# Performance work log

Measured on AMD Instinct MI355X. Metric: run time of the kernel, lower is better.

## Reference

```python
import jax, jax.numpy as jnp
import numpy as np

N = 100000   # nodes
E = 1600000  # edges (avg degree 16)
D = 128      # input channels
H = 128      # hidden channels
BN_EPS = 1e-5

def setup_inputs() -> dict:
    key = jax.random.key(0)
    ks = jax.random.split(key, 8)
    x = jax.random.normal(ks[0], (N, D), dtype=jnp.float32)
    edge_index = jax.random.randint(ks[1], (2, E), 0, N, dtype=jnp.int32)
    s = 0.02
    W1 = jax.random.normal(ks[2], (D, H), dtype=jnp.float32) * s
    b1 = jnp.zeros((H,), jnp.float32)
    g1 = jnp.ones((H,), jnp.float32)   # BN gamma
    be1 = jnp.zeros((H,), jnp.float32) # BN beta
    W2 = jax.random.normal(ks[3], (H, H), dtype=jnp.float32) * s
    b2 = jnp.zeros((H,), jnp.float32)
    g2 = jnp.ones((H,), jnp.float32)
    be2 = jnp.zeros((H,), jnp.float32)
    eps = jnp.zeros((), jnp.float32)   # trainable GIN eps, init 0
    return {"x": x, "edge_index": edge_index, "W1": W1, "b1": b1, "g1": g1,
            "be1": be1, "W2": W2, "b2": b2, "g2": g2, "be2": be2, "eps": eps}

def _bn_relu(h, gamma, beta):
    # BatchNorm1d in training mode: biased batch statistics over the node dim
    mu = jnp.mean(h, axis=0)
    var = jnp.mean(jnp.square(h - mu), axis=0)
    return jax.nn.relu((h - mu) * jax.lax.rsqrt(var + BN_EPS) * gamma + beta)

def reference(x, edge_index, W1, b1, g1, be1, W2, b2, g2, be2, eps):
    src, dst = edge_index[0], edge_index[1]
    # GIN neighbor aggregation: scatter-add of source features onto destinations
    agg = jax.ops.segment_sum(x[src], dst, num_segments=x.shape[0])  # [N, D]
    h = (1.0 + eps) * x + agg
    # 2-layer MLP: Linear -> BN -> ReLU, twice
    h = _bn_relu(h @ W1 + b1, g1, be1)
    h = _bn_relu(h @ W2 + b2, g2, be2)
    return h
```

## Files before the change

### kernel.cpp

```cpp
#include <hip/hip_runtime.h>

#define DIM 128
#define BINSHIFT 7
#define BINSZ 128
#define BCAP 2560
#define EPB 8192

typedef __attribute__((ext_vector_type(8))) short bf16x8;
typedef __attribute__((ext_vector_type(4))) float f32x4;

__device__ inline unsigned short f2b(float f) {
    unsigned u = __builtin_bit_cast(unsigned, f);
    unsigned r = (u + 0x7FFFu + ((u >> 16) & 1u)) >> 16;
    return (unsigned short)r;
}
__device__ inline float b2f(unsigned short h) {
    unsigned u = ((unsigned)h) << 16;
    return __builtin_bit_cast(float, u);
}

__global__ __launch_bounds__(256)
void x_to_bf16z(const float* __restrict__ x, unsigned short* __restrict__ xb,
                unsigned* __restrict__ zbuf, int n8)
{
    if (blockIdx.x == 0) {
        #pragma unroll
        for (int q = 0; q < 6; ++q) zbuf[threadIdx.x + q * 256] = 0u;
    }
    int i = blockIdx.x * 256 + threadIdx.x;
    if (i >= n8) return;
    float4 a = ((const float4*)x)[i * 2];
    float4 b = ((const float4*)x)[i * 2 + 1];
    bf16x8 o;
    o[0] = (short)f2b(a.x); o[1] = (short)f2b(a.y); o[2] = (short)f2b(a.z); o[3] = (short)f2b(a.w);
    o[4] = (short)f2b(b.x); o[5] = (short)f2b(b.y); o[6] = (short)f2b(b.z); o[7] = (short)f2b(b.w);
    ((bf16x8*)xb)[i] = o;
}

__global__ __launch_bounds__(1024)
void bin_edges(const int* __restrict__ src, const int* __restrict__ dst,
               unsigned* __restrict__ gcur, unsigned* __restrict__ binned,
               int E, int nbins)
{
    __shared__ unsigned hist[1024];
    __shared__ unsigned base[1024];
    const int t = threadIdx.x;
    const long long bb = (long long)blockIdx.x * EPB;
    if (t < nbins) hist[t] = 0;
    __syncthreads();

    unsigned pk[8], pos[8];
    int bn[8];
    bool ok[8];
    #pragma unroll
    for (int i = 0; i < 8; ++i) {
        long long idx = bb + i * 1024 + t;
        ok[i] = idx < E;
        if (ok[i]) {
            int s = src[idx], d = dst[idx];
            pk[i] = ((unsigned)(d & (BINSZ - 1)) << 17) | (unsigned)s;
            bn[i] = d >> BINSHIFT;
            pos[i] = atomicAdd(&hist[bn[i]], 1u);
        }
    }
    __syncthreads();
    if (t < nbins) base[t] = (unsigned)t * BCAP + atomicAdd(&gcur[t], hist[t]);
    __syncthreads();
    #pragma unroll
    for (int i = 0; i < 8; ++i) {
        if (ok[i]) {
            unsigned off = base[bn[i]] + pos[i];
            if (off < (unsigned)(bn[i] + 1) * BCAP) binned[off] = pk[i];
        }
    }
}

__global__ __launch_bounds__(512)
void bin_sort(const unsigned* __restrict__ gcur, const unsigned* __restrict__ binned,
              unsigned* __restrict__ srt, unsigned* __restrict__ gbase,
              unsigned* __restrict__ ghist)
{
    __shared__ unsigned hist[BINSZ];
    __shared__ unsigned base[BINSZ];
    __shared__ unsigned cur[BINSZ];
    const int t = threadIdx.x;
    const int bin = blockIdx.x;

    if (t < BINSZ) hist[t] = 0;
    __syncthreads();

    int cnt = (int)gcur[bin];
    if (cnt > BCAP) cnt = BCAP;
    const unsigned* __restrict__ bp = binned + (size_t)bin * BCAP;

    for (int i = t; i < cnt; i += 512)
        atomicAdd(&hist[(bp[i] >> 17) & (BINSZ - 1)], 1u);
    __syncthreads();
    if (t == 0) {
        unsigned run = 0;
        for (int i = 0; i < BINSZ; ++i) { base[i] = run; run += hist[i]; }
    }
    __syncthreads();
    if (t < BINSZ) cur[t] = base[t];
    __syncthreads();
    unsigned* __restrict__ sp = srt + (size_t)bin * BCAP;
    for (int i = t; i < cnt; i += 512) {
        unsigned p = bp[i];
        unsigned pos = atomicAdd(&cur[(p >> 17) & (BINSZ - 1)], 1u);
        sp[pos] = p & 0x1FFFFu;
    }
    if (t < BINSZ) {
        gbase[bin * BINSZ + t] = base[t];
        ghist[bin * BINSZ + t] = hist[t];
    }
}

__global__ __launch_bounds__(512)
void gather_csr(const unsigned short* __restrict__ xb, const float* __restrict__ epsp,
                const unsigned* __restrict__ srt, const unsigned* __restrict__ gbase,
                const unsigned* __restrict__ ghist,
                unsigned short* __restrict__ h0b, int N)
{
    const int t = threadIdx.x;
    const int node = blockIdx.x * 32 + (t >> 4);
    if (node >= N) return;
    const int g = (t & 15) * 8;
    const float e = 1.0f + epsp[0];

    bf16x8 v0 = *(const bf16x8*)(xb + (size_t)node * DIM + g);
    float acc[8];
    #pragma unroll
    for (int q = 0; q < 8; ++q) acc[q] = e * b2f((unsigned short)v0[q]);

    const int b0 = (int)gbase[node];
    const int hn = (int)ghist[node];
    const unsigned* __restrict__ sp = srt + (size_t)(node >> BINSHIFT) * BCAP + b0;

    int j = 0;
    for (; j + 8 <= hn; j += 8) {
        unsigned s0 = sp[j+0], s1 = sp[j+1], s2 = sp[j+2], s3 = sp[j+3];
        unsigned s4 = sp[j+4], s5 = sp[j+5], s6 = sp[j+6], s7 = sp[j+7];
        bf16x8 r0 = *(const bf16x8*)(xb + (size_t)s0 * DIM + g);
        bf16x8 r1 = *(const bf16x8*)(xb + (size_t)s1 * DIM + g);
        bf16x8 r2 = *(const bf16x8*)(xb + (size_t)s2 * DIM + g);
        bf16x8 r3 = *(const bf16x8*)(xb + (size_t)s3 * DIM + g);
        bf16x8 r4 = *(const bf16x8*)(xb + (size_t)s4 * DIM + g);
        bf16x8 r5 = *(const bf16x8*)(xb + (size_t)s5 * DIM + g);
        bf16x8 r6 = *(const bf16x8*)(xb + (size_t)s6 * DIM + g);
        bf16x8 r7 = *(const bf16x8*)(xb + (size_t)s7 * DIM + g);
        #pragma unroll
        for (int q = 0; q < 8; ++q)
            acc[q] += b2f((unsigned short)r0[q]) + b2f((unsigned short)r1[q])
                    + b2f((unsigned short)r2[q]) + b2f((unsigned short)r3[q])
                    + b2f((unsigned short)r4[q]) + b2f((unsigned short)r5[q])
                    + b2f((unsigned short)r6[q]) + b2f((unsigned short)r7[q]);
    }
    for (; j + 2 <= hn; j += 2) {
        unsigned s0 = sp[j+0], s1 = sp[j+1];
        bf16x8 r0 = *(const bf16x8*)(xb + (size_t)s0 * DIM + g);
        bf16x8 r1 = *(const bf16x8*)(xb + (size_t)s1 * DIM + g);
        #pragma unroll
        for (int q = 0; q < 8; ++q)
            acc[q] += b2f((unsigned short)r0[q]) + b2f((unsigned short)r1[q]);
    }
    for (; j < hn; ++j) {
        unsigned s0 = sp[j];
        bf16x8 r0 = *(const bf16x8*)(xb + (size_t)s0 * DIM + g);
        #pragma unroll
        for (int q = 0; q < 8; ++q) acc[q] += b2f((unsigned short)r0[q]);
    }
    bf16x8 o;
    #pragma unroll
    for (int q = 0; q < 8; ++q) o[q] = (short)f2b(acc[q]);
    *(bf16x8*)(h0b + (size_t)node * DIM + g) = o;
}

template<bool APPLY_BN, bool OUT_BF16>
__global__ __launch_bounds__(1024)
void gemm_mfma(const unsigned short* __restrict__ A, const float* __restrict__ Wf,
               const float* __restrict__ bias,
               const float* __restrict__ stats_in, const float* __restrict__ gamma,
               const float* __restrict__ beta, float invN,
               void* __restrict__ outp, float* __restrict__ stats, int N)
{
    __shared__ unsigned short sWT[128 * 128];
    __shared__ float red[256];
    __shared__ float sss[256];
    const int tid = threadIdx.x;

    if (APPLY_BN && tid < 128) {
        float mu  = stats_in[tid] * invN;
        float var = fmaxf(stats_in[128 + tid] * invN - mu * mu, 0.f);
        float sc  = gamma[tid] * rsqrtf(var + 1e-5f);
        sss[tid]       = sc;
        sss[128 + tid] = beta[tid] - mu * sc;
    }
    #pragma unroll
    for (int i = 0; i < 4; ++i) {
        int idx = (i * 1024 + tid) * 4;
        float4 w = *(const float4*)&Wf[idx];
        int k = idx >> 7, n0 = idx & 127;
        sWT[(n0 + 0) * 128 + (k ^ (((n0 + 0) & 7) << 3))] = f2b(w.x);
        sWT[(n0 + 1) * 128 + (k ^ (((n0 + 1) & 7) << 3))] = f2b(w.y);
        sWT[(n0 + 2) * 128 + (k ^ (((n0 + 2) & 7) << 3))] = f2b(w.z);
        sWT[(n0 + 3) * 128 + (k ^ (((n0 + 3) & 7) << 3))] = f2b(w.w);
    }
    if (tid < 256) red[tid] = 0.f;
    __syncthreads();

    const int lane = tid & 63;
    const int wave = tid >> 6;
    const int r0   = blockIdx.x * 256 + wave * 16;
    const int rl   = lane & 15;
    const int kg   = lane >> 4;
    int rr = r0 + rl;
    int rclamp = rr < N ? rr : N - 1;
    const unsigned short* arow = A + (size_t)rclamp * DIM + kg * 8;

    f32x4 acc[8];
    #pragma unroll
    for (int nt = 0; nt < 8; ++nt) acc[nt] = (f32x4)(0.f);

    #pragma unroll
    for (int kk = 0; kk < 128; kk += 32) {
        bf16x8 a8 = *(const bf16x8*)(arow + kk);
        if (APPLY_BN) {
            const int cb = kk + kg * 8;
            bf16x8 tt;
            #pragma unroll
            for (int j = 0; j < 8; ++j) {
                float f = b2f((unsigned short)a8[j]) * sss[cb + j] + sss[128 + cb + j];
                tt[j] = (short)f2b(fmaxf(f, 0.f));
            }
            a8 = tt;
        }
        const int ks = kk + kg * 8;
        #pragma unroll
        for (int nt = 0; nt < 8; ++nt) {
            int n = nt * 16 + rl;
            bf16x8 b8 = *(const bf16x8*)&sWT[n * 128 + (ks ^ ((n & 7) << 3))];
            acc[nt] = __builtin_amdgcn_mfma_f32_16x16x32_bf16(a8, b8, acc[nt], 0, 0, 0);
        }
    }

    const int orow0 = r0 + kg * 4;
    #pragma unroll
    for (int nt = 0; nt < 8; ++nt) {
        int n = nt * 16 + rl;
        float bb = bias[n];
        float ls = 0.f, ls2 = 0.f;
        #pragma unroll
        for (int j = 0; j < 4; ++j) {
            int r = orow0 + j;
            if (r < N) {
                float v = acc[nt][j] + bb;
                if (OUT_BF16) ((unsigned short*)outp)[(size_t)r * DIM + n] = f2b(v);
                else          ((float*)outp)[(size_t)r * DIM + n] = v;
                ls += v; ls2 += v * v;
            }
        }
        ls  += __shfl_xor(ls, 16);  ls  += __shfl_xor(ls, 32);
        ls2 += __shfl_xor(ls2, 16); ls2 += __shfl_xor(ls2, 32);
        if (kg == 0) { atomicAdd(&red[n], ls); atomicAdd(&red[128 + n], ls2); }
    }
    __syncthreads();
    if (tid < 256) atomicAdd(&stats[tid], red[tid]);
}

__global__ __launch_bounds__(256)
void bn_relu_out_b(const unsigned short* __restrict__ h2b,
                   const float* __restrict__ stats, const float* __restrict__ gamma,
                   const float* __restrict__ beta, float invN,
                   float* __restrict__ out, int n8)
{
    __shared__ float sss[256];
    const int tid = threadIdx.x;
    if (tid < 128) {
        float mu  = stats[tid] * invN;
        float var = fmaxf(stats[128 + tid] * invN - mu * mu, 0.f);
        float sc  = gamma[tid] * rsqrtf(var + 1e-5f);
        sss[tid]       = sc;
        sss[128 + tid] = beta[tid] - mu * sc;
    }
    __syncthreads();
    int i = blockIdx.x * 256 + tid;
    if (i >= n8) return;
    int c = (i * 8) & 127;
    bf16x8 v = *(const bf16x8*)(h2b + (size_t)i * 8);
    float4 o0, o1;
    o0.x = fmaxf(b2f((unsigned short)v[0]) * sss[c+0] + sss[128+c+0], 0.f);
    o0.y = fmaxf(b2f((unsigned short)v[1]) * sss[c+1] + sss[128+c+1], 0.f);
    o0.z = fmaxf(b2f((unsigned short)v[2]) * sss[c+2] + sss[128+c+2], 0.f);
    o0.w = fmaxf(b2f((unsigned short)v[3]) * sss[c+3] + sss[128+c+3], 0.f);
    o1.x = fmaxf(b2f((unsigned short)v[4]) * sss[c+4] + sss[128+c+4], 0.f);
    o1.y = fmaxf(b2f((unsigned short)v[5]) * sss[c+5] + sss[128+c+5], 0.f);
    o1.z = fmaxf(b2f((unsigned short)v[6]) * sss[c+6] + sss[128+c+6], 0.f);
    o1.w = fmaxf(b2f((unsigned short)v[7]) * sss[c+7] + sss[128+c+7], 0.f);
    ((float4*)out)[i * 2 + 0] = o0;
    ((float4*)out)[i * 2 + 1] = o1;
}

extern "C" void kernel_launch(void* const* d_in, const int* in_sizes, int n_in,
                              void* d_out, int out_size, void* d_ws, size_t ws_size,
                              hipStream_t stream) {
    const float* x    = (const float*)d_in[0];
    const int*   ei   = (const int*)  d_in[1];
    const float* W1   = (const float*)d_in[2];
    const float* b1   = (const float*)d_in[3];
    const float* g1   = (const float*)d_in[4];
    const float* be1  = (const float*)d_in[5];
    const float* W2   = (const float*)d_in[6];
    const float* b2   = (const float*)d_in[7];
    const float* g2   = (const float*)d_in[8];
    const float* be2  = (const float*)d_in[9];
    const float* epsp = (const float*)d_in[10];
    float* out = (float*)d_out;

    const int N = in_sizes[0] / DIM;
    const int E = in_sizes[1] / 2;
    const int* src = ei;
    const int* dst = ei + E;
    const int nbins = (N + BINSZ - 1) >> BINSHIFT;

    const size_t SZ = (size_t)N * DIM * sizeof(unsigned short);
    char* w = (char*)d_ws;
    unsigned short* xb  = (unsigned short*)w;
    unsigned short* h0b = (unsigned short*)(w + SZ);
    unsigned short* h2b = h0b;
    unsigned short* h1b = (unsigned short*)(w + 2 * SZ);
    unsigned* binned = (unsigned*)(w + 2 * SZ);
    unsigned* srt    = binned + (size_t)nbins * BCAP;
    unsigned* gbase  = srt + (size_t)nbins * BCAP;
    unsigned* ghist  = gbase + (size_t)nbins * BINSZ;
    unsigned* gcur   = (unsigned*)(w + 3 * SZ);
    float* stats1 = (float*)(gcur + 1024);
    float* stats2 = stats1 + 256;

    const float invN = 1.0f / (float)N;
    const int n8 = N * DIM / 8;

    x_to_bf16z<<<(n8 + 255) / 256, 256, 0, stream>>>(x, xb, gcur, n8);
    bin_edges<<<(E + EPB - 1) / EPB, 1024, 0, stream>>>(src, dst, gcur, binned, E, nbins);
    bin_sort<<<nbins, 512, 0, stream>>>(gcur, binned, srt, gbase, ghist);
    gather_csr<<<(N + 31) / 32, 512, 0, stream>>>(xb, epsp, srt, gbase, ghist, h0b, N);

    const int gblocks = (N + 255) / 256;
    gemm_mfma<false, true><<<gblocks, 1024, 0, stream>>>(
        h0b, W1, b1, nullptr, nullptr, nullptr, invN, h1b, stats1, N);
    gemm_mfma<true, true><<<gblocks, 1024, 0, stream>>>(
        h1b, W2, b2, stats1, g1, be1, invN, h2b, stats2, N);
    bn_relu_out_b<<<(n8 + 255) / 256, 256, 0, stream>>>(h2b, stats2, g2, be2, invN, out, n8);
}
```

Measured before the change: 187.8 us.

## Fuse edge binning with bf16 cast, parallelize bin scan, shorten gather unroll

The x-to-bf16 conversion and edge binning now run in a single launch, with blocks split by index, and the zeroing of counters moves to a hipMemsetAsync. The serial prefix sum in bin_sort is replaced by a wavefront shuffle scan over 128 entries. The gather loop unroll drops from 8 to 4 neighbors, which lowers register pressure but gives less memory-level parallelism. The GEMM template loses its unused fp32 output path.

```diff
diff --git a/kernel.cpp b/kernel.cpp
--- a/kernel.cpp
+++ b/kernel.cpp
@@ -19,59 +19,52 @@
     return __builtin_bit_cast(float, u);
 }
 
-__global__ __launch_bounds__(256)
-void x_to_bf16z(const float* __restrict__ x, unsigned short* __restrict__ xb,
-                unsigned* __restrict__ zbuf, int n8)
-{
-    if (blockIdx.x == 0) {
-        #pragma unroll
-        for (int q = 0; q < 6; ++q) zbuf[threadIdx.x + q * 256] = 0u;
-    }
-    int i = blockIdx.x * 256 + threadIdx.x;
-    if (i >= n8) return;
-    float4 a = ((const float4*)x)[i * 2];
-    float4 b = ((const float4*)x)[i * 2 + 1];
-    bf16x8 o;
-    o[0] = (short)f2b(a.x); o[1] = (short)f2b(a.y); o[2] = (short)f2b(a.z); o[3] = (short)f2b(a.w);
-    o[4] = (short)f2b(b.x); o[5] = (short)f2b(b.y); o[6] = (short)f2b(b.z); o[7] = (short)f2b(b.w);
-    ((bf16x8*)xb)[i] = o;
-}
-
 __global__ __launch_bounds__(1024)
-void bin_edges(const int* __restrict__ src, const int* __restrict__ dst,
-               unsigned* __restrict__ gcur, unsigned* __restrict__ binned,
-               int E, int nbins)
-{
-    __shared__ unsigned hist[1024];
-    __shared__ unsigned base[1024];
+void prep(const int* __restrict__ src, const int* __restrict__ dst,
+          unsigned* __restrict__ gcur, unsigned* __restrict__ binned, int E, int nbins,
+          const float* __restrict__ x, unsigned short* __restrict__ xb, int n8, int ebB)
+{
     const int t = threadIdx.x;
-    const long long bb = (long long)blockIdx.x * EPB;
-    if (t < nbins) hist[t] = 0;
-    __syncthreads();
-
-    unsigned pk[8], pos[8];
-    int bn[8];
-    bool ok[8];
-    #pragma unroll
-    for (int i = 0; i < 8; ++i) {
-        long long idx = bb + i * 1024 + t;
-        ok[i] = idx < E;
-        if (ok[i]) {
-            int s = src[idx], d = dst[idx];
-            pk[i] = ((unsigned)(d & (BINSZ - 1)) << 17) | (unsigned)s;
-            bn[i] = d >> BINSHIFT;
-            pos[i] = atomicAdd(&hist[bn[i]], 1u);
-        }
-    }
-    __syncthreads();
-    if (t < nbins) base[t] = (unsigned)t * BCAP + atomicAdd(&gcur[t], hist[t]);
-    __syncthreads();
-    #pragma unroll
-    for (int i = 0; i < 8; ++i) {
-        if (ok[i]) {
-            unsigned off = base[bn[i]] + pos[i];
-            if (off < (unsigned)(bn[i] + 1) * BCAP) binned[off] = pk[i];
-        }
+    const int bid = blockIdx.x;
+    if (bid < ebB) {
+        __shared__ unsigned hist[1024];
+        __shared__ unsigned base[1024];
+        const long long bb = (long long)bid * EPB;
+        if (t < nbins) hist[t] = 0;
+        __syncthreads();
+        unsigned pk[8], pos[8];
+        int bn[8];
+        bool ok[8];
+        #pragma unroll
+        for (int i = 0; i < 8; ++i) {
+            long long idx = bb + i * 1024 + t;
+            ok[i] = idx < E;
+            if (ok[i]) {
+                int s = src[idx], d = dst[idx];
+                pk[i] = ((unsigned)(d & (BINSZ - 1)) << 17) | (unsigned)s;
+                bn[i] = d >> BINSHIFT;
+                pos[i] = atomicAdd(&hist[bn[i]], 1u);
+            }
+        }
+        __syncthreads();
+        if (t < nbins) base[t] = (unsigned)t * BCAP + atomicAdd(&gcur[t], hist[t]);
+        __syncthreads();
+        #pragma unroll
+        for (int i = 0; i < 8; ++i) {
+            if (ok[i]) {
+                unsigned off = base[bn[i]] + pos[i];
+                if (off < (unsigned)(bn[i] + 1) * BCAP) binned[off] = pk[i];
+            }
+        }
+    } else {
+        int i = (bid - ebB) * 1024 + t;
+        if (i >= n8) return;
+        float4 a = ((const float4*)x)[i * 2];
+        float4 b = ((const float4*)x)[i * 2 + 1];
+        bf16x8 o;
+        o[0] = (short)f2b(a.x); o[1] = (short)f2b(a.y); o[2] = (short)f2b(a.z); o[3] = (short)f2b(a.w);
+        o[4] = (short)f2b(b.x); o[5] = (short)f2b(b.y); o[6] = (short)f2b(b.z); o[7] = (short)f2b(b.w);
+        ((bf16x8*)xb)[i] = o;
     }
 }
 
@@ -83,6 +76,7 @@
     __shared__ unsigned hist[BINSZ];
     __shared__ unsigned base[BINSZ];
     __shared__ unsigned cur[BINSZ];
+    __shared__ unsigned wtot_s;
     const int t = threadIdx.x;
     const int bin = blockIdx.x;
 
@@ -96,12 +90,23 @@
     for (int i = t; i < cnt; i += 512)
         atomicAdd(&hist[(bp[i] >> 17) & (BINSZ - 1)], 1u);
     __syncthreads();
-    if (t == 0) {
-        unsigned run = 0;
-        for (int i = 0; i < BINSZ; ++i) { base[i] = run; run += hist[i]; }
-    }
-    __syncthreads();
-    if (t < BINSZ) cur[t] = base[t];
+    unsigned iv = 0, hv = 0;
+    if (t < BINSZ) {
+        hv = hist[t];
+        iv = hv;
+        #pragma unroll
+        for (int d = 1; d < 64; d <<= 1) {
+            unsigned u = __shfl_up(iv, d);
+            if ((t & 63) >= d) iv += u;
+        }
+        if (t == 63) wtot_s = iv;
+    }
+    __syncthreads();
+    if (t < BINSZ) {
+        unsigned ex = iv - hv + ((t >= 64) ? wtot_s : 0u);
+        base[t] = ex;
+        cur[t] = ex;
+    }
     __syncthreads();
     unsigned* __restrict__ sp = srt + (size_t)bin * BCAP;
     for (int i = t; i < cnt; i += 512) {
@@ -137,31 +142,19 @@
     const unsigned* __restrict__ sp = srt + (size_t)(node >> BINSHIFT) * BCAP + b0;
 
     int j = 0;
-    for (; j + 8 <= hn; j += 8) {
-        unsigned s0 = sp[j+0], s1 = sp[j+1], s2 = sp[j+2], s3 = sp[j+3];
-        unsigned s4 = sp[j+4], s5 = sp[j+5], s6 = sp[j+6], s7 = sp[j+7];
+    for (; j + 4 <= hn; j += 4) {
+        unsigned s0 = sp[j + 0];
+        unsigned s1 = sp[j + 1];
+        unsigned s2 = sp[j + 2];
+        unsigned s3 = sp[j + 3];
         bf16x8 r0 = *(const bf16x8*)(xb + (size_t)s0 * DIM + g);
         bf16x8 r1 = *(const bf16x8*)(xb + (size_t)s1 * DIM + g);
         bf16x8 r2 = *(const bf16x8*)(xb + (size_t)s2 * DIM + g);
         bf16x8 r3 = *(const bf16x8*)(xb + (size_t)s3 * DIM + g);
-        bf16x8 r4 = *(const bf16x8*)(xb + (size_t)s4 * DIM + g);
-        bf16x8 r5 = *(const bf16x8*)(xb + (size_t)s5 * DIM + g);
-        bf16x8 r6 = *(const bf16x8*)(xb + (size_t)s6 * DIM + g);
-        bf16x8 r7 = *(const bf16x8*)(xb + (size_t)s7 * DIM + g);
         #pragma unroll
         for (int q = 0; q < 8; ++q)
             acc[q] += b2f((unsigned short)r0[q]) + b2f((unsigned short)r1[q])
-                    + b2f((unsigned short)r2[q]) + b2f((unsigned short)r3[q])
-                    + b2f((unsigned short)r4[q]) + b2f((unsigned short)r5[q])
-                    + b2f((unsigned short)r6[q]) + b2f((unsigned short)r7[q]);
-    }
-    for (; j + 2 <= hn; j += 2) {
-        unsigned s0 = sp[j+0], s1 = sp[j+1];
-        bf16x8 r0 = *(const bf16x8*)(xb + (size_t)s0 * DIM + g);
-        bf16x8 r1 = *(const bf16x8*)(xb + (size_t)s1 * DIM + g);
-        #pragma unroll
-        for (int q = 0; q < 8; ++q)
-            acc[q] += b2f((unsigned short)r0[q]) + b2f((unsigned short)r1[q]);
+                    + b2f((unsigned short)r2[q]) + b2f((unsigned short)r3[q]);
     }
     for (; j < hn; ++j) {
         unsigned s0 = sp[j];
@@ -175,13 +168,13 @@
     *(bf16x8*)(h0b + (size_t)node * DIM + g) = o;
 }
 
-template<bool APPLY_BN, bool OUT_BF16>
+template<bool APPLY_BN>
 __global__ __launch_bounds__(1024)
 void gemm_mfma(const unsigned short* __restrict__ A, const float* __restrict__ Wf,
                const float* __restrict__ bias,
                const float* __restrict__ stats_in, const float* __restrict__ gamma,
                const float* __restrict__ beta, float invN,
-               void* __restrict__ outp, float* __restrict__ stats, int N)
+               unsigned short* __restrict__ outp, float* __restrict__ stats, int N)
 {
     __shared__ unsigned short sWT[128 * 128];
     __shared__ float red[256];
@@ -254,8 +247,7 @@
             int r = orow0 + j;
             if (r < N) {
                 float v = acc[nt][j] + bb;
-                if (OUT_BF16) ((unsigned short*)outp)[(size_t)r * DIM + n] = f2b(v);
-                else          ((float*)outp)[(size_t)r * DIM + n] = v;
+                outp[(size_t)r * DIM + n] = f2b(v);
                 ls += v; ls2 += v * v;
             }
         }
@@ -338,16 +330,17 @@
 
     const float invN = 1.0f / (float)N;
     const int n8 = N * DIM / 8;
-
-    x_to_bf16z<<<(n8 + 255) / 256, 256, 0, stream>>>(x, xb, gcur, n8);
-    bin_edges<<<(E + EPB - 1) / EPB, 1024, 0, stream>>>(src, dst, gcur, binned, E, nbins);
+    const int ebB = (E + EPB - 1) / EPB;
+    const int castB = (n8 + 1023) / 1024;
+
+    hipMemsetAsync(gcur, 0, (1024 + 512) * sizeof(unsigned), stream);
+    prep<<<ebB + castB, 1024, 0, stream>>>(src, dst, gcur, binned, E, nbins, x, xb, n8, ebB);
     bin_sort<<<nbins, 512, 0, stream>>>(gcur, binned, srt, gbase, ghist);
     gather_csr<<<(N + 31) / 32, 512, 0, stream>>>(xb, epsp, srt, gbase, ghist, h0b, N);
-
     const int gblocks = (N + 255) / 256;
-    gemm_mfma<false, true><<<gblocks, 1024, 0, stream>>>(
+    gemm_mfma<false><<<gblocks, 1024, 0, stream>>>(
         h0b, W1, b1, nullptr, nullptr, nullptr, invN, h1b, stats1, N);
-    gemm_mfma<true, true><<<gblocks, 1024, 0, stream>>>(
+    gemm_mfma<true><<<gblocks, 1024, 0, stream>>>(
         h1b, W2, b2, stats1, g1, be1, invN, h2b, stats2, N);
     bn_relu_out_b<<<(n8 + 255) / 256, 256, 0, stream>>>(h2b, stats2, g2, be2, invN, out, n8);
 }
```

After: 185.1 us. Within noise of the previous version (-1.4%).
